# Optimization experiments

Hardware: AMD Instinct MI355X
Metric: run time of the kernel (lower is better)

The kernel has to match this reference:

```python
import jax, jax.numpy as jnp
import numpy as np

B, S, HID = 4, 2048, 2048
H, KV, D = 16, 4, 128
ROT = 32  # partial rotary dim
EPS = 1e-6
NEG = -1e9


def _rms_norm(x, w):
    # Qwen3-Next RMSNorm: fp32 norm, (1 + weight) scaling
    xf = x.astype(jnp.float32)
    out = xf * jax.lax.rsqrt(jnp.mean(xf * xf, axis=-1, keepdims=True) + EPS)
    return (out * (1.0 + w.astype(jnp.float32))).astype(x.dtype)


def _rotate_half(x):
    x1, x2 = x[..., : x.shape[-1] // 2], x[..., x.shape[-1] // 2 :]
    return jnp.concatenate((-x2, x1), axis=-1)


def setup_inputs() -> dict:
    key = jax.random.key(0)
    ks = jax.random.split(key, 8)
    hidden_states = jax.random.normal(ks[0], (B, S, HID), dtype=jnp.float32)
    # real RoPE angles for the partial rotary dims
    inv_freq = 1.0 / (10000.0 ** (np.arange(0, ROT, 2, dtype=np.float32) / ROT))
    pos = np.arange(S, dtype=np.float32)
    freqs = np.einsum('s,d->sd', pos, inv_freq)          # [S, ROT/2]
    emb = np.concatenate([freqs, freqs], axis=-1)         # [S, ROT]
    cos = jnp.broadcast_to(jnp.asarray(np.cos(emb)), (B, S, ROT))
    sin = jnp.broadcast_to(jnp.asarray(np.sin(emb)), (B, S, ROT))
    # additive causal mask [B,1,S,S]
    causal = jnp.triu(jnp.full((S, S), NEG, dtype=jnp.float32), k=1)
    attention_mask = jnp.broadcast_to(causal[None, None], (B, 1, S, S))
    std = 0.02
    wq = jax.random.normal(ks[1], (HID, H * D * 2), dtype=jnp.float32) * std
    wk = jax.random.normal(ks[2], (HID, KV * D), dtype=jnp.float32) * std
    wv = jax.random.normal(ks[3], (HID, KV * D), dtype=jnp.float32) * std
    wo = jax.random.normal(ks[4], (H * D, HID), dtype=jnp.float32) * std
    q_norm_w = jax.random.normal(ks[5], (D,), dtype=jnp.float32) * std
    k_norm_w = jax.random.normal(ks[6], (D,), dtype=jnp.float32) * std
    return {
        'hidden_states': hidden_states, 'cos': cos, 'sin': sin,
        'attention_mask': attention_mask, 'wq': wq, 'wk': wk, 'wv': wv,
        'wo': wo, 'q_norm_w': q_norm_w, 'k_norm_w': k_norm_w,
    }


def reference(hidden_states, cos, sin, attention_mask, wq, wk, wv, wo, q_norm_w, k_norm_w):
    b, s, _ = hidden_states.shape
    scaling = D ** -0.5
    # q projection -> [B,S,H,2D]; split into query and gate (chunk dim=-1)
    qg = (hidden_states @ wq).reshape(b, s, H, 2 * D)
    q, gate = qg[..., :D], qg[..., D:]
    gate = gate.reshape(b, s, H * D)
    q = _rms_norm(q, q_norm_w).transpose(0, 2, 1, 3)                    # [B,H,S,D]
    k = _rms_norm((hidden_states @ wk).reshape(b, s, KV, D), k_norm_w).transpose(0, 2, 1, 3)
    v = (hidden_states @ wv).reshape(b, s, KV, D).transpose(0, 2, 1, 3)  # [B,KV,S,D]
    # partial RoPE on first ROT dims
    c, sn = cos[:, None], sin[:, None]                                   # [B,1,S,ROT]
    q_rot, q_pass = q[..., :ROT], q[..., ROT:]
    k_rot, k_pass = k[..., :ROT], k[..., ROT:]
    q = jnp.concatenate([q_rot * c + _rotate_half(q_rot) * sn, q_pass], axis=-1)
    k = jnp.concatenate([k_rot * c + _rotate_half(k_rot) * sn, k_pass], axis=-1)
    # GQA: repeat kv heads
    groups = H // KV
    k = jnp.repeat(k, groups, axis=1)
    v = jnp.repeat(v, groups, axis=1)
    scores = jnp.einsum('bhqd,bhkd->bhqk', q, k) * scaling + attention_mask
    probs = jax.nn.softmax(scores.astype(jnp.float32), axis=-1).astype(q.dtype)
    attn = jnp.einsum('bhqk,bhkd->bhqd', probs, v)
    attn = attn.transpose(0, 2, 1, 3).reshape(b, s, H * D)
    attn = attn * jax.nn.sigmoid(gate)
    return attn @ wo
```

## Files before the change

### kernel.cpp

```cpp
#include <hip/hip_runtime.h>

#define SEQ   2048
#define NHEAD 16
#define NKV   4
#define HDIM  128
#define NB    4
#define QKVW  5120

typedef unsigned short u16;
typedef unsigned int   u32;
typedef __bf16 v8bf __attribute__((ext_vector_type(8)));
typedef float  v4f  __attribute__((ext_vector_type(4)));

__device__ __forceinline__ u16 f2bf(float f) {
  u32 u = __float_as_uint(f);
  u += 0x7fffu + ((u >> 16) & 1u);
  return (u16)(u >> 16);
}
__device__ __forceinline__ float bf2f(u16 b) {
  return __uint_as_float(((u32)b) << 16);
}

__device__ __forceinline__ void gld_lds16(const u16* g, u16* l) {
  __builtin_amdgcn_global_load_lds(
      (const __attribute__((address_space(1))) u32*)(unsigned long long)(uintptr_t)g,
      (__attribute__((address_space(3))) u32*)(u32)(uintptr_t)l,
      16, 0, 0);
}

__device__ __forceinline__ void conv_body(const float* __restrict__ s,
                                          u16* __restrict__ d, int blk, int t) {
  size_t i = ((size_t)blk * 256 + t) * 8;
  float4 a = *(const float4*)(s + i);
  float4 b = *(const float4*)(s + i + 4);
  uint4 o;
  o.x = (u32)f2bf(a.x) | ((u32)f2bf(a.y) << 16);
  o.y = (u32)f2bf(a.z) | ((u32)f2bf(a.w) << 16);
  o.z = (u32)f2bf(b.x) | ((u32)f2bf(b.y) << 16);
  o.w = (u32)f2bf(b.z) | ((u32)f2bf(b.w) << 16);
  *(uint4*)(d + i) = o;
}

__device__ __forceinline__ void tw_body(const float* __restrict__ src,
                                        u16* __restrict__ dst, int R, int C,
                                        int bx, int by, int t,
                                        u16 (*tile)[80]) {
  int r0 = by * 64, c0 = bx * 64;
  int rr = t >> 2, cc = (t & 3) * 16;
  const float* sp = src + (size_t)(r0 + rr) * C + c0 + cc;
  float4 f0 = *(const float4*)sp;
  float4 f1 = *(const float4*)(sp + 4);
  float4 f2 = *(const float4*)(sp + 8);
  float4 f3 = *(const float4*)(sp + 12);
  u16* tp = &tile[rr][cc];
  tp[0] = f2bf(f0.x);  tp[1] = f2bf(f0.y);  tp[2] = f2bf(f0.z);  tp[3] = f2bf(f0.w);
  tp[4] = f2bf(f1.x);  tp[5] = f2bf(f1.y);  tp[6] = f2bf(f1.z);  tp[7] = f2bf(f1.w);
  tp[8] = f2bf(f2.x);  tp[9] = f2bf(f2.y);  tp[10] = f2bf(f2.z); tp[11] = f2bf(f2.w);
  tp[12] = f2bf(f3.x); tp[13] = f2bf(f3.y); tp[14] = f2bf(f3.z); tp[15] = f2bf(f3.w);
  __syncthreads();
  int cr = t >> 2, rc = (t & 3) * 16;
  u32 pk[8];
#pragma unroll
  for (int i = 0; i < 8; i++) {
    u32 lo = tile[rc + 2 * i][cr];
    u32 hi = tile[rc + 2 * i + 1][cr];
    pk[i] = lo | (hi << 16);
  }
  u16* dp = dst + (size_t)(c0 + cr) * R + r0 + rc;
  uint4 o0 = {pk[0], pk[1], pk[2], pk[3]};
  uint4 o1 = {pk[4], pk[5], pk[6], pk[7]};
  *(uint4*)dp       = o0;
  *(uint4*)(dp + 8) = o1;
}

__device__ __forceinline__ void tv_body(const u16* __restrict__ qkv,
                                        u16* __restrict__ vt,
                                        int sx, int dy, int bg, int t,
                                        u16 (*tile)[80]) {
  int s0 = sx * 64;
  int d0 = dy * 64;
  int b = bg >> 2, g = bg & 3;
  int sr = t >> 2, dc = (t & 3) * 16;
  const u16* sp = qkv + (size_t)(b * SEQ + s0 + sr) * QKVW + 4608 + g * HDIM + d0 + dc;
  *(uint4*)&tile[sr][dc]     = *(const uint4*)sp;
  *(uint4*)&tile[sr][dc + 8] = *(const uint4*)(sp + 8);
  __syncthreads();
  int dr = t >> 2, sc = (t & 3) * 16;
  u32 pk[8];
#pragma unroll
  for (int i = 0; i < 8; i++) {
    u32 lo = tile[sc + 2 * i][dr];
    u32 hi = tile[sc + 2 * i + 1][dr];
    pk[i] = lo | (hi << 16);
  }
  u16* dp = vt + ((size_t)bg * HDIM + d0 + dr) * SEQ + s0 + sc;
  uint4 o0 = {pk[0], pk[1], pk[2], pk[3]};
  uint4 o1 = {pk[4], pk[5], pk[6], pk[7]};
  *(uint4*)dp       = o0;
  *(uint4*)(dp + 8) = o1;
}

__device__ __forceinline__ void nr_body(u16* __restrict__ qkv,
                                        const float* __restrict__ cosb,
                                        const float* __restrict__ sinb,
                                        const float* __restrict__ qw,
                                        const float* __restrict__ kw,
                                        u16* __restrict__ kf,
                                        int blk, int tidx) {
  int wave = tidx >> 6, lane = tidx & 63;
  int tw = blk * 4 + wave;
  int token = tw / 20, r = tw % 20;
  const u16* src;
  u16* dst;
  const float* wptr;
  if (r < 16) {
    src  = qkv + (size_t)token * QKVW + r * 256;
    dst  = (u16*)src;
    wptr = qw;
  } else {
    src  = qkv + (size_t)token * QKVW + 4096 + (r - 16) * HDIM;
    int b = token >> 11, s = token & (SEQ - 1);
    dst  = kf + ((size_t)(b * NKV + (r - 16)) * SEQ + s) * HDIM;
    wptr = kw;
  }
  int d0 = lane * 2;
  u32 x = *(const u32*)(src + d0);
  float x0 = bf2f((u16)(x & 0xffff)), x1 = bf2f((u16)(x >> 16));
  float ss = x0 * x0 + x1 * x1;
#pragma unroll
  for (int off = 1; off < 64; off <<= 1) ss += __shfl_xor(ss, off, 64);
  float sc = rsqrtf(ss * (1.f / 128.f) + 1e-6f);
  float y0 = bf2f(f2bf(x0 * sc * (1.f + wptr[d0])));
  float y1 = bf2f(f2bf(x1 * sc * (1.f + wptr[d0 + 1])));
  float p0 = __shfl_xor(y0, 8, 64);
  float p1 = __shfl_xor(y1, 8, 64);
  float z0 = y0, z1 = y1;
  if (lane < 16) {
    float c0 = cosb[(size_t)token * 32 + d0];
    float c1 = cosb[(size_t)token * 32 + d0 + 1];
    float s0 = sinb[(size_t)token * 32 + d0];
    float s1 = sinb[(size_t)token * 32 + d0 + 1];
    if (lane < 8) { z0 = y0 * c0 - p0 * s0; z1 = y1 * c1 - p1 * s1; }
    else          { z0 = y0 * c0 + p0 * s0; z1 = y1 * c1 + p1 * s1; }
  }
  u32 outp = (u32)f2bf(z0) | ((u32)f2bf(z1) << 16);
  *(u32*)(dst + d0) = outp;
}

__global__ __launch_bounds__(256) void prep0(const float* __restrict__ hidden,
                                             u16* __restrict__ hidden_bf,
                                             const float* __restrict__ wq,
                                             const float* __restrict__ wk,
                                             const float* __restrict__ wv,
                                             u16* __restrict__ bt_qkv) {
  __shared__ u16 tile[64][80];
  int b = blockIdx.x, t = threadIdx.x;
  if (b < 8192) {
    conv_body(hidden, hidden_bf, b, t);
  } else if (b < 10240) {
    int idx = b - 8192;
    tw_body(wq, bt_qkv, 2048, 4096, idx & 63, idx >> 6, t, tile);
  } else if (b < 10496) {
    int idx = b - 10240;
    tw_body(wk, bt_qkv + (size_t)4096 * 2048, 2048, 512, idx & 7, idx >> 3, t, tile);
  } else {
    int idx = b - 10496;
    tw_body(wv, bt_qkv + (size_t)4608 * 2048, 2048, 512, idx & 7, idx >> 3, t, tile);
  }
}

__global__ __launch_bounds__(256) void prep1(u16* __restrict__ qkv,
                                             const float* __restrict__ cosb,
                                             const float* __restrict__ sinb,
                                             const float* __restrict__ qw,
                                             const float* __restrict__ kw,
                                             u16* __restrict__ kf,
                                             u16* __restrict__ vt,
                                             const float* __restrict__ wo,
                                             u16* __restrict__ bt_wo) {
  __shared__ u16 tile[64][80];
  int b = blockIdx.x, t = threadIdx.x;
  if (b < 40960) {
    nr_body(qkv, cosb, sinb, qw, kw, kf, b, t);
  } else if (b < 41984) {
    int idx = b - 40960;
    tv_body(qkv, vt, idx & 31, (idx >> 5) & 1, idx >> 6, t, tile);
  } else {
    int idx = b - 41984;
    tw_body(wo, bt_wo, 2048, 2048, idx & 31, idx >> 5, t, tile);
  }
}

template <bool OUT_F32>
__global__ __launch_bounds__(512, 2) void gemm_bt(const u16* __restrict__ A,
                                                  const u16* __restrict__ Bt,
                                                  void* __restrict__ Cp,
                                                  int M, int N, int K) {
  __shared__ u16 As[3][256 * 32];
  __shared__ u16 Bs[3][256 * 32];
  int tid  = threadIdx.x;
  int lane = tid & 63, wave = tid >> 6;
  int wr = wave >> 2, wc = wave & 3;
  int col = lane & 15, quad = lane >> 4;
  int nwg = gridDim.x;
  int cpx = nwg >> 3;
  int id  = blockIdx.x;
  int idp = (id & 7) * cpx + (id >> 3);
  int ntile = N >> 8;
  int m0 = (idp / ntile) << 8;
  int n0 = (idp % ntile) << 8;

  v4f acc[8][4];
#pragma unroll
  for (int mi = 0; mi < 8; mi++)
#pragma unroll
    for (int ni = 0; ni < 4; ni++) acc[mi][ni] = (v4f){0.f, 0.f, 0.f, 0.f};

  int srow = tid >> 2;
  int skc  = (tid & 3) * 8;
  const u16* ag = A  + (size_t)(m0 + srow) * K + skc;
  const u16* bg = Bt + (size_t)(n0 + srow) * K + skc;
  const size_t rowK128 = (size_t)128 * K;

#define STAGE(buf, k0)                                        \
  do {                                                        \
    gld_lds16(ag + (k0),           &As[buf][tid * 8]);        \
    gld_lds16(ag + rowK128 + (k0), &As[buf][4096 + tid * 8]); \
    gld_lds16(bg + (k0),           &Bs[buf][tid * 8]);        \
    gld_lds16(bg + rowK128 + (k0), &Bs[buf][4096 + tid * 8]); \
  } while (0)

  STAGE(0, 0);
  STAGE(1, 32);
  asm volatile("s_waitcnt vmcnt(4)\n\ts_barrier" ::: "memory");

  const int NT = K >> 5;
  int cb = 0;
  for (int t = 0; t < NT; ++t) {
    int sb = cb + 2 >= 3 ? cb - 1 : cb + 2;
    if (t + 2 < NT) {
      int k0 = (t + 2) << 5;
      STAGE(sb, k0);
    }
    v8bf bfr[4];
#pragma unroll
    for (int ni = 0; ni < 4; ni++)
      bfr[ni] = *(const v8bf*)&Bs[cb][(wc * 64 + ni * 16 + col) * 32 + quad * 8];
    __builtin_amdgcn_s_setprio(1);
#pragma unroll
    for (int mi = 0; mi < 8; mi++) {
      v8bf a = *(const v8bf*)&As[cb][(wr * 128 + mi * 16 + col) * 32 + quad * 8];
#pragma unroll
      for (int ni = 0; ni < 4; ni++)
        acc[mi][ni] = __builtin_amdgcn_mfma_f32_16x16x32_bf16(a, bfr[ni], acc[mi][ni], 0, 0, 0);
    }
    __builtin_amdgcn_s_setprio(0);
    if (t < NT - 2) asm volatile("s_waitcnt vmcnt(4)\n\ts_barrier" ::: "memory");
    else            asm volatile("s_waitcnt vmcnt(0)\n\ts_barrier" ::: "memory");
    cb = cb + 1 >= 3 ? 0 : cb + 1;
  }
#undef STAGE

#pragma unroll
  for (int mi = 0; mi < 8; mi++)
#pragma unroll
    for (int ni = 0; ni < 4; ni++) {
      int r_ = m0 + wr * 128 + mi * 16 + quad * 4;
      int c_ = n0 + wc * 64 + ni * 16 + col;
#pragma unroll
      for (int r = 0; r < 4; r++) {
        if (OUT_F32) ((float*)Cp)[(size_t)(r_ + r) * N + c_] = acc[mi][ni][r];
        else         ((u16*)Cp)[(size_t)(r_ + r) * N + c_]   = f2bf(acc[mi][ni][r]);
      }
    }
}

__global__ __launch_bounds__(512) void attn_kernel(const u16* __restrict__ qkv,
                                                   const u16* __restrict__ kf,
                                                   const u16* __restrict__ vt,
                                                   u16* __restrict__ ga) {
  __shared__ u16 ks[64 * 136];
  __shared__ u16 vs[128 * 88];
  int tid = threadIdx.x, lane = tid & 63, wave = tid >> 6;
  int col = lane & 15, quad = lane >> 4;
  int qt = 15 - blockIdx.x;
  int h = blockIdx.y, b = blockIdx.z;
  int g = h >> 2;
  int qw0 = qt * 128 + wave * 16;
  int myq = qw0 + col;
  const float scl2 = 0.08838834764831845f * 1.4426950408889634f;

  v8bf qfr[4];
  const u16* qbase = qkv + (size_t)(b * SEQ + myq) * QKVW + h * 256 + quad * 8;
#pragma unroll
  for (int kc = 0; kc < 4; kc++) qfr[kc] = *(const v8bf*)(qbase + kc * 32);

  v4f o[8];
#pragma unroll
  for (int nt = 0; nt < 8; nt++) o[nt] = (v4f){0.f, 0.f, 0.f, 0.f};
  float l = 0.f;
  float m = -1e30f;

  const u16* kfb = kf + (size_t)(b * NKV + g) * SEQ * HDIM;
  const u16* vtb = vt + (size_t)(b * NKV + g) * HDIM * SEQ;

  int ksr = tid >> 4, ksd = (tid & 15) * 8;
  int vsd = tid >> 3, w8 = tid & 7;
  int voff = 32 * ((w8 >> 2) & 1) + 16 * (w8 & 1) + 4 * ((w8 >> 1) & 1);
  int vsrc = w8 * 8;

  int nk = 2 * qt + 2;
  for (int it = 0; it < nk; it++) {
    int k0 = it * 64;
    __syncthreads();
#pragma unroll
    for (int p = 0; p < 2; p++)
      *(uint4*)&ks[(p * 32 + ksr) * 136 + ksd] =
          *(const uint4*)&kfb[(size_t)(k0 + p * 32 + ksr) * HDIM + ksd];
#pragma unroll
    for (int p = 0; p < 2; p++) {
      int d = p * 64 + vsd;
      uint4 gv = *(const uint4*)&vtb[(size_t)d * SEQ + k0 + vsrc];
      uint2 w0 = {gv.x, gv.y};
      uint2 w1 = {gv.z, gv.w};
      *(uint2*)&vs[d * 88 + voff]     = w0;
      *(uint2*)&vs[d * 88 + voff + 8] = w1;
    }
    __syncthreads();

    v4f st[4];
    __builtin_amdgcn_s_setprio(1);
#pragma unroll
    for (int t = 0; t < 4; t++) {
      v4f acc = (v4f){0.f, 0.f, 0.f, 0.f};
#pragma unroll
      for (int kc = 0; kc < 4; kc++) {
        v8bf kfr = *(const v8bf*)&ks[(t * 16 + col) * 136 + kc * 32 + quad * 8];
        acc = __builtin_amdgcn_mfma_f32_16x16x32_bf16(kfr, qfr[kc], acc, 0, 0, 0);
      }
      st[t] = acc;
    }
    __builtin_amdgcn_s_setprio(0);

    bool maskw = (k0 + 63 > qw0);
    float pmax = -1e30f;
#pragma unroll
    for (int t = 0; t < 4; t++)
#pragma unroll
      for (int r = 0; r < 4; r++) {
        float x = st[t][r] * scl2;
        if (maskw && (k0 + t * 16 + quad * 4 + r > myq)) x = -1e30f;
        st[t][r] = x;
        pmax = fmaxf(pmax, x);
      }
    pmax = fmaxf(pmax, __shfl_xor(pmax, 16, 64));
    pmax = fmaxf(pmax, __shfl_xor(pmax, 32, 64));
    if (__any(pmax > m + 8.f)) {
      float nm = fmaxf(m, pmax);
      float al = exp2f(m - nm);
      m = nm;
#pragma unroll
      for (int nt = 0; nt < 8; nt++)
#pragma unroll
        for (int r = 0; r < 4; r++) o[nt][r] *= al;
      l *= al;
    }
    v8bf pb0, pb1;
    float ls = 0.f;
#pragma unroll
    for (int t = 0; t < 4; t++)
#pragma unroll
      for (int r = 0; r < 4; r++) {
        float p = exp2f(st[t][r] - m);
        ls += p;
        if (t < 2) pb0[t * 4 + r] = (__bf16)p;
        else       pb1[(t - 2) * 4 + r] = (__bf16)p;
      }
    l += ls;

    __builtin_amdgcn_s_setprio(1);
#pragma unroll
    for (int nt = 0; nt < 8; nt++) {
      v8bf vb0 = *(const v8bf*)&vs[(nt * 16 + col) * 88 + quad * 8];
      v8bf vb1 = *(const v8bf*)&vs[(nt * 16 + col) * 88 + 32 + quad * 8];
      o[nt] = __builtin_amdgcn_mfma_f32_16x16x32_bf16(vb0, pb0, o[nt], 0, 0, 0);
      o[nt] = __builtin_amdgcn_mfma_f32_16x16x32_bf16(vb1, pb1, o[nt], 0, 0, 0);
    }
    __builtin_amdgcn_s_setprio(0);
  }

  l += __shfl_xor(l, 16, 64);
  l += __shfl_xor(l, 32, 64);
  float inv = 1.f / l;
  const u16* gb = qkv + (size_t)(b * SEQ + myq) * QKVW + h * 256 + 128 + quad * 4;
  u16* ob = ga + (size_t)(b * SEQ + myq) * 2048 + h * HDIM + quad * 4;
#pragma unroll
  for (int nt = 0; nt < 8; nt++) {
    uint2 gw = *(const uint2*)(gb + nt * 16);
    float g0 = bf2f((u16)(gw.x & 0xffff)), g1 = bf2f((u16)(gw.x >> 16));
    float g2 = bf2f((u16)(gw.y & 0xffff)), g3 = bf2f((u16)(gw.y >> 16));
    float a0 = o[nt][0] * inv * (1.f / (1.f + expf(-g0)));
    float a1 = o[nt][1] * inv * (1.f / (1.f + expf(-g1)));
    float a2 = o[nt][2] * inv * (1.f / (1.f + expf(-g2)));
    float a3 = o[nt][3] * inv * (1.f / (1.f + expf(-g3)));
    uint2 ow;
    ow.x = (u32)f2bf(a0) | ((u32)f2bf(a1) << 16);
    ow.y = (u32)f2bf(a2) | ((u32)f2bf(a3) << 16);
    *(uint2*)(ob + nt * 16) = ow;
  }
}

extern "C" void kernel_launch(void* const* d_in, const int* in_sizes, int n_in,
                              void* d_out, int out_size, void* d_ws, size_t ws_size,
                              hipStream_t stream) {
  const float* hidden = (const float*)d_in[0];
  const float* cosb   = (const float*)d_in[1];
  const float* sinb   = (const float*)d_in[2];
  const float* wq  = (const float*)d_in[4];
  const float* wk  = (const float*)d_in[5];
  const float* wv  = (const float*)d_in[6];
  const float* wo  = (const float*)d_in[7];
  const float* qnw = (const float*)d_in[8];
  const float* knw = (const float*)d_in[9];
  float* out = (float*)d_out;

  u16* ws      = (u16*)d_ws;
  u16* qkv_raw = ws;
  u16* region2 = qkv_raw + (size_t)8192 * QKVW;
  u16* region3 = region2 + (size_t)8192 * 2048;
  u16* hidden_bf = region2;
  u16* g_attn    = region2;
  u16* bt_qkv    = region3;
  u16* vt        = region3;
  u16* bt_wo     = region3 + (size_t)4194304;
  u16* k_f       = region3 + (size_t)8388608;

  prep0<<<dim3(10752), 256, 0, stream>>>(hidden, hidden_bf, wq, wk, wv, bt_qkv);
  gemm_bt<false><<<dim3(640), 512, 0, stream>>>(hidden_bf, bt_qkv, qkv_raw, 8192, QKVW, 2048);
  prep1<<<dim3(43008), 256, 0, stream>>>(qkv_raw, cosb, sinb, qnw, knw, k_f, vt, wo, bt_wo);
  attn_kernel<<<dim3(16, NHEAD, NB), 512, 0, stream>>>(qkv_raw, k_f, vt, g_attn);
  gemm_bt<true><<<dim3(256), 512, 0, stream>>>(g_attn, bt_wo, out, 8192, 2048, 2048);
}
```

Before: 674.7 us.

## Double-buffer attention K/V tiles with async global-to-LDS loads and XOR swizzle

Replaces the synchronous register-staged K/V tile loads in the attention kernel with direct global-to-LDS loads into two LDS buffers. The next tile is prefetched while the current one is being computed, and one wait-plus-barrier per iteration replaces the two syncthreads. The padded LDS layout is swapped for an XOR-swizzled unpadded layout to avoid bank conflicts. The cost is double the LDS footprint and V fragments now assembled from four 8-byte reads, with correctness depending on the swizzle indexing matching the permuted V layout.

```diff
diff --git a/kernel.cpp b/kernel.cpp
--- a/kernel.cpp
+++ b/kernel.cpp
@@ -26,6 +26,12 @@
       (const __attribute__((address_space(1))) u32*)(unsigned long long)(uintptr_t)g,
       (__attribute__((address_space(3))) u32*)(u32)(uintptr_t)l,
       16, 0, 0);
+}
+
+__device__ __forceinline__ v8bf mkv8(uint2 a, uint2 b) {
+  union { u32 w[4]; v8bf v; } u;
+  u.w[0] = a.x; u.w[1] = a.y; u.w[2] = b.x; u.w[3] = b.y;
+  return u.v;
 }
 
 __device__ __forceinline__ void conv_body(const float* __restrict__ s,
@@ -279,8 +285,8 @@
                                                    const u16* __restrict__ kf,
                                                    const u16* __restrict__ vt,
                                                    u16* __restrict__ ga) {
-  __shared__ u16 ks[64 * 136];
-  __shared__ u16 vs[128 * 88];
+  __shared__ u16 ks[2][64 * 128];
+  __shared__ u16 vs[2][128 * 64];
   int tid = threadIdx.x, lane = tid & 63, wave = tid >> 6;
   int col = lane & 15, quad = lane >> 4;
   int qt = 15 - blockIdx.x;
@@ -304,29 +310,30 @@
   const u16* kfb = kf + (size_t)(b * NKV + g) * SEQ * HDIM;
   const u16* vtb = vt + (size_t)(b * NKV + g) * HDIM * SEQ;
 
-  int ksr = tid >> 4, ksd = (tid & 15) * 8;
-  int vsd = tid >> 3, w8 = tid & 7;
-  int voff = 32 * ((w8 >> 2) & 1) + 16 * (w8 & 1) + 4 * ((w8 >> 1) & 1);
-  int vsrc = w8 * 8;
+  int kRow0 = tid >> 4;
+  int kDoff = ((tid & 15) ^ ((tid >> 4) & 7)) * 8;
+  const u16* kSrc0 = kfb + (size_t)kRow0 * HDIM + kDoff;
+  int vRow0 = tid >> 3;
+  int vKoff = (((tid & 7) ^ ((tid >> 3) & 7)) * 8);
+  const u16* vSrc0 = vtb + (size_t)vRow0 * SEQ + vKoff;
+
+#define ASTAGE(db, kq)                                            \
+  do {                                                            \
+    const u16* ksrc = kSrc0 + (size_t)(kq) * HDIM;                \
+    gld_lds16(ksrc,             &ks[db][tid * 8]);                \
+    gld_lds16(ksrc + 32 * HDIM, &ks[db][4096 + tid * 8]);         \
+    const u16* vsrc = vSrc0 + (kq);                               \
+    gld_lds16(vsrc,             &vs[db][tid * 8]);                \
+    gld_lds16(vsrc + 64 * SEQ,  &vs[db][4096 + tid * 8]);         \
+  } while (0)
 
   int nk = 2 * qt + 2;
+  ASTAGE(0, 0);
+  int db = 0;
   for (int it = 0; it < nk; it++) {
     int k0 = it * 64;
-    __syncthreads();
-#pragma unroll
-    for (int p = 0; p < 2; p++)
-      *(uint4*)&ks[(p * 32 + ksr) * 136 + ksd] =
-          *(const uint4*)&kfb[(size_t)(k0 + p * 32 + ksr) * HDIM + ksd];
-#pragma unroll
-    for (int p = 0; p < 2; p++) {
-      int d = p * 64 + vsd;
-      uint4 gv = *(const uint4*)&vtb[(size_t)d * SEQ + k0 + vsrc];
-      uint2 w0 = {gv.x, gv.y};
-      uint2 w1 = {gv.z, gv.w};
-      *(uint2*)&vs[d * 88 + voff]     = w0;
-      *(uint2*)&vs[d * 88 + voff + 8] = w1;
-    }
-    __syncthreads();
+    asm volatile("s_waitcnt vmcnt(0)\n\ts_barrier" ::: "memory");
+    if (it + 1 < nk) ASTAGE(db ^ 1, k0 + 64);
 
     v4f st[4];
     __builtin_amdgcn_s_setprio(1);
@@ -335,7 +342,8 @@
       v4f acc = (v4f){0.f, 0.f, 0.f, 0.f};
 #pragma unroll
       for (int kc = 0; kc < 4; kc++) {
-        v8bf kfr = *(const v8bf*)&ks[(t * 16 + col) * 136 + kc * 32 + quad * 8];
+        v8bf kfr = *(const v8bf*)&ks[db][(t * 16 + col) * 128 +
+                                         (((kc * 4 + quad) ^ (col & 7)) * 8)];
         acc = __builtin_amdgcn_mfma_f32_16x16x32_bf16(kfr, qfr[kc], acc, 0, 0, 0);
       }
       st[t] = acc;
@@ -378,16 +386,24 @@
       }
     l += ls;
 
+    int sw = (col & 7) * 8;
     __builtin_amdgcn_s_setprio(1);
 #pragma unroll
     for (int nt = 0; nt < 8; nt++) {
-      v8bf vb0 = *(const v8bf*)&vs[(nt * 16 + col) * 88 + quad * 8];
-      v8bf vb1 = *(const v8bf*)&vs[(nt * 16 + col) * 88 + 32 + quad * 8];
+      int vrow = (nt * 16 + col) * 64;
+      uint2 c0 = *(const uint2*)&vs[db][vrow + ((quad * 4) ^ sw)];
+      uint2 c1 = *(const uint2*)&vs[db][vrow + ((16 + quad * 4) ^ sw)];
+      uint2 c2 = *(const uint2*)&vs[db][vrow + ((32 + quad * 4) ^ sw)];
+      uint2 c3 = *(const uint2*)&vs[db][vrow + ((48 + quad * 4) ^ sw)];
+      v8bf vb0 = mkv8(c0, c1);
+      v8bf vb1 = mkv8(c2, c3);
       o[nt] = __builtin_amdgcn_mfma_f32_16x16x32_bf16(vb0, pb0, o[nt], 0, 0, 0);
       o[nt] = __builtin_amdgcn_mfma_f32_16x16x32_bf16(vb1, pb1, o[nt], 0, 0, 0);
     }
     __builtin_amdgcn_s_setprio(0);
-  }
+    db ^= 1;
+  }
+#undef ASTAGE
 
   l += __shfl_xor(l, 16, 64);
   l += __shfl_xor(l, 32, 64);
```

Result: slower. 724.9 us (+7.4%).
